# Optimization experiments

Measured on AMD Instinct MI355X. Metric: run time of the kernel, lower is better.

Reference implementation:

```python
import jax, jax.numpy as jnp
import numpy as np


def setup_inputs() -> dict:
    key = jax.random.key(0)
    k1, k2, k3 = jax.random.split(key, 3)
    B, T, H, OUT = 32, 2048, 1024, 256
    hidden_states = jax.random.normal(k1, (B, T, H), dtype=jnp.float32)
    W1 = jax.random.normal(k2, (H, H), dtype=jnp.float32) * (1.0 / np.sqrt(H))
    b1 = jnp.zeros((H,), dtype=jnp.float32)
    Wv = jax.random.normal(k3, (2 * H, OUT), dtype=jnp.float32) * (1.0 / np.sqrt(2 * H))
    bv = jnp.zeros((OUT,), dtype=jnp.float32)
    return {"hidden_states": hidden_states, "W1": W1, "b1": b1, "Wv": Wv, "bv": bv}


def reference(hidden_states, W1, b1, Wv, bv):
    # first_score = Dense(H)(hidden_states): [B,T,H]
    first_score = jnp.einsum('bth,hk->btk', hidden_states, W1) + b1
    # h_t = last timestep of the PROJECTED states: [B,H]
    h_t = first_score[:, -1, :]
    # score = dot([first_score, h_t], [2,1]): [B,T]
    score = jnp.einsum('bth,bh->bt', first_score, h_t)
    attention_weights = jax.nn.softmax(score, axis=-1)  # softmax over T
    # context = dot([hidden_states, weights], [1,1]): contract T -> [B,H]
    context_vector = jnp.einsum('bth,bt->bh', hidden_states, attention_weights)
    pre_activation = jnp.concatenate([context_vector, h_t], axis=-1)  # [B,2H]
    return jnp.tanh(pre_activation @ Wv + bv)  # [B,256]
```

## Files before the change

kernel.cpp:

```cpp
#include <hip/hip_runtime.h>
#include <math.h>

#define B   32
#define T   2048
#define H   1024
#define OUTD 256
#define NC  32
#define KC1 16

__global__ __launch_bounds__(256) void k1a_partial_ht(
    const float* __restrict__ hs, const float* __restrict__ W1,
    float* __restrict__ ph)
{
    const int tid = threadIdx.x;
    const int h   = blockIdx.x * 256 + tid;
    const int k0  = blockIdx.y * 64;

    __shared__ float s_hs[B][64];
    for (int it = 0; it < 8; ++it) {
        int idx = tid + it * 256;
        int b = idx >> 6, k = idx & 63;
        s_hs[b][k] = hs[((size_t)(b * T + (T - 1)) << 10) + k0 + k];
    }
    __syncthreads();

    float acc[B];
#pragma unroll
    for (int b = 0; b < B; ++b) acc[b] = 0.f;

    for (int k4 = 0; k4 < 16; ++k4) {
        float w0 = W1[(size_t)(k0 + k4 * 4 + 0) * H + h];
        float w1 = W1[(size_t)(k0 + k4 * 4 + 1) * H + h];
        float w2 = W1[(size_t)(k0 + k4 * 4 + 2) * H + h];
        float w3 = W1[(size_t)(k0 + k4 * 4 + 3) * H + h];
#pragma unroll
        for (int b = 0; b < B; ++b) {
            const float4 hv = *(const float4*)&s_hs[b][k4 * 4];
            acc[b] = fmaf(hv.x, w0, acc[b]);
            acc[b] = fmaf(hv.y, w1, acc[b]);
            acc[b] = fmaf(hv.z, w2, acc[b]);
            acc[b] = fmaf(hv.w, w3, acc[b]);
        }
    }
    float* dst = ph + ((size_t)blockIdx.y * B << 10);
#pragma unroll
    for (int b = 0; b < B; ++b) dst[((size_t)b << 10) + h] = acc[b];
}

__global__ __launch_bounds__(256) void k1b_reduce_ht(
    const float* __restrict__ ph, const float* __restrict__ b1,
    float* __restrict__ h_t)
{
    int i = blockIdx.x * 256 + threadIdx.x;
    int h = i & (H - 1);
    float s = b1[h];
#pragma unroll
    for (int c = 0; c < KC1; ++c)
        s += ph[((size_t)c * B << 10) + i];
    h_t[i] = s;
}

__global__ __launch_bounds__(256) void k2_compute_u(
    const float* __restrict__ W1, const float* __restrict__ h_t,
    float* __restrict__ u)
{
    const int wid  = threadIdx.x >> 6;
    const int lane = threadIdx.x & 63;
    const int k    = blockIdx.x * 4 + wid;
    const float4* wr = (const float4*)(W1 + ((size_t)k << 10));
    float4 wq[4];
#pragma unroll
    for (int j = 0; j < 4; ++j) wq[j] = wr[lane + 64 * j];

    for (int b = 0; b < B; ++b) {
        const float4* hr = (const float4*)(h_t + ((size_t)b << 10));
        float s = 0.f;
#pragma unroll
        for (int j = 0; j < 4; ++j) {
            float4 hv = hr[lane + 64 * j];
            s += wq[j].x * hv.x + wq[j].y * hv.y + wq[j].z * hv.z + wq[j].w * hv.w;
        }
#pragma unroll
        for (int off = 32; off; off >>= 1) s += __shfl_xor(s, off, 64);
        if (lane == 0) u[((size_t)b << 10) + k] = s;
    }
}

__global__ __launch_bounds__(256) void k3_fused(
    const float* __restrict__ hs, const float* __restrict__ u,
    float* __restrict__ ctx_p, float* __restrict__ m_p, float* __restrict__ l_p)
{
    const int c    = blockIdx.x;
    const int b    = blockIdx.y;
    const int w    = threadIdx.x >> 6;
    const int lane = threadIdx.x & 63;
    const int tid  = threadIdx.x;

    const float4* urow = (const float4*)(u + ((size_t)b << 10));
    float4 uq[4];
#pragma unroll
    for (int j = 0; j < 4; ++j) uq[j] = urow[lane + 64 * j];

    const int t0 = c * 64 + w * 16;
    const float4* xrow = (const float4*)(hs + ((size_t)(b * T + t0) << 10));

    float m = -INFINITY, lsum = 0.f;
    float4 acc[4];
#pragma unroll
    for (int j = 0; j < 4; ++j) acc[j] = make_float4(0.f, 0.f, 0.f, 0.f);

    float4 x[4], y[4];
#pragma unroll
    for (int j = 0; j < 4; ++j) x[j] = xrow[lane + 64 * j];

    for (int r = 0; r < 16; ++r) {
        const float4* nrow = xrow + 256;
        if (r < 15) {
#pragma unroll
            for (int j = 0; j < 4; ++j) y[j] = nrow[lane + 64 * j];
        }
        float s = 0.f;
#pragma unroll
        for (int j = 0; j < 4; ++j)
            s += x[j].x * uq[j].x + x[j].y * uq[j].y + x[j].z * uq[j].z + x[j].w * uq[j].w;
#pragma unroll
        for (int off = 32; off; off >>= 1) s += __shfl_xor(s, off, 64);

        float mn = fmaxf(m, s);
        float al = __expf(m - mn);
        float wt = __expf(s - mn);
        lsum = lsum * al + wt;
#pragma unroll
        for (int j = 0; j < 4; ++j) {
            acc[j].x = fmaf(acc[j].x, al, wt * x[j].x);
            acc[j].y = fmaf(acc[j].y, al, wt * x[j].y);
            acc[j].z = fmaf(acc[j].z, al, wt * x[j].z);
            acc[j].w = fmaf(acc[j].w, al, wt * x[j].w);
        }
        m = mn;
#pragma unroll
        for (int j = 0; j < 4; ++j) x[j] = y[j];
        xrow = nrow;
    }

    __shared__ float sm[4], sl[4];
    __shared__ float sacc[4][H];
    if (lane == 0) { sm[w] = m; sl[w] = lsum; }
    __syncthreads();
    const float mp = fmaxf(fmaxf(sm[0], sm[1]), fmaxf(sm[2], sm[3]));
    const float alw = __expf(m - mp);
    float4* sa = (float4*)&sacc[w][0];
#pragma unroll
    for (int j = 0; j < 4; ++j) {
        float4 v;
        v.x = acc[j].x * alw; v.y = acc[j].y * alw;
        v.z = acc[j].z * alw; v.w = acc[j].w * alw;
        sa[lane + 64 * j] = v;
    }
    __syncthreads();
    float lp = 0.f;
#pragma unroll
    for (int ww = 0; ww < 4; ++ww) lp += sl[ww] * __expf(sm[ww] - mp);

    float* dst = ctx_p + (((size_t)b * NC + c) << 10);
#pragma unroll
    for (int i = 0; i < 4; ++i) {
        int h = tid + 256 * i;
        dst[h] = sacc[0][h] + sacc[1][h] + sacc[2][h] + sacc[3][h];
    }
    if (tid == 0) { m_p[b * NC + c] = mp; l_p[b * NC + c] = lp; }
}

__global__ __launch_bounds__(256) void k4_combine(
    const float* __restrict__ ctx_p, const float* __restrict__ m_p,
    const float* __restrict__ l_p, const float* __restrict__ h_t,
    float* __restrict__ pre)
{
    const int b   = blockIdx.x;
    const int tid = threadIdx.x;
    __shared__ float e[NC];
    float M = -INFINITY;
    for (int c = 0; c < NC; ++c) M = fmaxf(M, m_p[b * NC + c]);
    float L = 0.f;
    for (int c = 0; c < NC; ++c) L += l_p[b * NC + c] * __expf(m_p[b * NC + c] - M);
    if (tid < NC) e[tid] = __expf(m_p[b * NC + tid] - M);
    __syncthreads();
    const float inv = 1.f / L;
#pragma unroll
    for (int i = 0; i < 4; ++i) {
        int h = tid + 256 * i;
        float s = 0.f;
#pragma unroll
        for (int c = 0; c < NC; ++c)
            s += ctx_p[(((size_t)b * NC + c) << 10) + h] * e[c];
        pre[((size_t)b << 11) + h] = s * inv;
        pre[((size_t)b << 11) + H + h] = h_t[((size_t)b << 10) + h];
    }
}

__global__ __launch_bounds__(256) void k5a_matmul(
    const float* __restrict__ pre, const float* __restrict__ Wv,
    float* __restrict__ accum)
{
    const int kc = blockIdx.x;
    const int b  = blockIdx.y;
    const int o  = threadIdx.x;
    __shared__ float sp[256];
    sp[o] = pre[((size_t)b << 11) + kc * 256 + o];
    __syncthreads();
    float acc = 0.f;
    const float* wv = Wv + (size_t)kc * 256 * OUTD + o;
#pragma unroll 8
    for (int k = 0; k < 256; ++k)
        acc = fmaf(sp[k], wv[(size_t)k * OUTD], acc);
    atomicAdd(&accum[b * OUTD + o], acc);
}

__global__ __launch_bounds__(256) void k5b_tanh(
    const float* __restrict__ accum, const float* __restrict__ bv,
    float* __restrict__ out)
{
    int i = blockIdx.x * 256 + threadIdx.x;
    out[i] = tanhf(accum[i] + bv[i & (OUTD - 1)]);
}

extern "C" void kernel_launch(void* const* d_in, const int* in_sizes, int n_in,
                              void* d_out, int out_size, void* d_ws, size_t ws_size,
                              hipStream_t stream)
{
    const float* hs = (const float*)d_in[0];
    const float* W1 = (const float*)d_in[1];
    const float* b1 = (const float*)d_in[2];
    const float* Wv = (const float*)d_in[3];
    const float* bv = (const float*)d_in[4];
    float* out = (float*)d_out;
    float* ws  = (float*)d_ws;

    float* ph    = ws;
    float* h_t   = ph + (size_t)KC1 * B * H;
    float* u     = h_t + (size_t)B * H;
    float* m_p   = u + (size_t)B * H;
    float* l_p   = m_p + B * NC;
    float* ctx_p = l_p + B * NC;
    float* pre   = ctx_p + (size_t)B * NC * H;
    float* accum = pre + (size_t)B * 2 * H;

    hipMemsetAsync(accum, 0, B * OUTD * sizeof(float), stream);

    k1a_partial_ht<<<dim3(4, KC1), 256, 0, stream>>>(hs, W1, ph);
    k1b_reduce_ht<<<(B * H) / 256, 256, 0, stream>>>(ph, b1, h_t);
    k2_compute_u<<<H / 4, 256, 0, stream>>>(W1, h_t, u);
    k3_fused<<<dim3(NC, B), 256, 0, stream>>>(hs, u, ctx_p, m_p, l_p);
    k4_combine<<<B, 256, 0, stream>>>(ctx_p, m_p, l_p, h_t, pre);
    k5a_matmul<<<dim3(8, B), 256, 0, stream>>>(pre, Wv, accum);
    k5b_tanh<<<B, 256, 0, stream>>>(accum, bv, out);
}
```

Measured before the change: 436.3 us.

## Fuse all stages into one persistent cooperative kernel with grid syncs

Merges the seven separate kernels and the memset into a single cooperative kernel. Each stage becomes a grid-stride job loop, and stages are separated by grid-wide synchronisation. The grid is sized from occupancy times CU count, and shared memory is reused across stages. This is meant to remove per-launch overhead and inter-kernel gaps, in exchange for grid-sync costs and occupancy limits from the unified register and LDS footprint.

```diff
diff --git a/kernel.cpp b/kernel.cpp
--- a/kernel.cpp
+++ b/kernel.cpp
@@ -1,227 +1,233 @@
 #include <hip/hip_runtime.h>
+#include <hip/hip_cooperative_groups.h>
 #include <math.h>
 
-#define B   32
-#define T   2048
-#define H   1024
+namespace cg = cooperative_groups;
+
+#define B    32
+#define T    2048
+#define H    1024
 #define OUTD 256
-#define NC  32
-#define KC1 16
-
-__global__ __launch_bounds__(256) void k1a_partial_ht(
+#define NC   32
+#define KC1  16
+
+__global__ __launch_bounds__(256, 4) void mega(
     const float* __restrict__ hs, const float* __restrict__ W1,
-    float* __restrict__ ph)
+    const float* __restrict__ b1, const float* __restrict__ Wv,
+    const float* __restrict__ bv, float* __restrict__ out,
+    float* ws)
 {
+    cg::grid_group grid = cg::this_grid();
+    const int bid = blockIdx.x;
     const int tid = threadIdx.x;
-    const int h   = blockIdx.x * 256 + tid;
-    const int k0  = blockIdx.y * 64;
-
-    __shared__ float s_hs[B][64];
-    for (int it = 0; it < 8; ++it) {
-        int idx = tid + it * 256;
-        int b = idx >> 6, k = idx & 63;
-        s_hs[b][k] = hs[((size_t)(b * T + (T - 1)) << 10) + k0 + k];
-    }
-    __syncthreads();
-
-    float acc[B];
-#pragma unroll
-    for (int b = 0; b < B; ++b) acc[b] = 0.f;
-
-    for (int k4 = 0; k4 < 16; ++k4) {
-        float w0 = W1[(size_t)(k0 + k4 * 4 + 0) * H + h];
-        float w1 = W1[(size_t)(k0 + k4 * 4 + 1) * H + h];
-        float w2 = W1[(size_t)(k0 + k4 * 4 + 2) * H + h];
-        float w3 = W1[(size_t)(k0 + k4 * 4 + 3) * H + h];
-#pragma unroll
+    const int gsz = gridDim.x;
+
+    float* ph    = ws;
+    float* h_t   = ph + (size_t)KC1 * B * H;
+    float* u     = h_t + (size_t)B * H;
+    float* m_p   = u + (size_t)B * H;
+    float* l_p   = m_p + B * NC;
+    float* ctx_p = l_p + B * NC;
+    float* pre   = ctx_p + (size_t)B * NC * H;
+    float* accum = pre + (size_t)B * 2 * H;
+
+    __shared__ float smem[4 * H + 8];
+
+    for (int job = bid; job < 65; job += gsz) {
+        if (job < 64) {
+            const int hh = (job & 3) * 256 + tid;
+            const int k0 = (job >> 2) * 64;
+            float (*s_hs)[64] = (float (*)[64])smem;
+            for (int it = 0; it < 8; ++it) {
+                int idx = tid + it * 256;
+                int b = idx >> 6, k = idx & 63;
+                s_hs[b][k] = hs[((size_t)(b * T + (T - 1)) << 10) + k0 + k];
+            }
+            __syncthreads();
+            float acc[B];
+#pragma unroll
+            for (int b = 0; b < B; ++b) acc[b] = 0.f;
+            for (int k4 = 0; k4 < 16; ++k4) {
+                float w0 = W1[(size_t)(k0 + k4 * 4 + 0) * H + hh];
+                float w1 = W1[(size_t)(k0 + k4 * 4 + 1) * H + hh];
+                float w2 = W1[(size_t)(k0 + k4 * 4 + 2) * H + hh];
+                float w3 = W1[(size_t)(k0 + k4 * 4 + 3) * H + hh];
+#pragma unroll
+                for (int b = 0; b < B; ++b) {
+                    const float4 hv = *(const float4*)&s_hs[b][k4 * 4];
+                    acc[b] = fmaf(hv.x, w0, acc[b]);
+                    acc[b] = fmaf(hv.y, w1, acc[b]);
+                    acc[b] = fmaf(hv.z, w2, acc[b]);
+                    acc[b] = fmaf(hv.w, w3, acc[b]);
+                }
+            }
+            float* dst = ph + ((size_t)(job >> 2) * B << 10);
+#pragma unroll
+            for (int b = 0; b < B; ++b) dst[((size_t)b << 10) + hh] = acc[b];
+            __syncthreads();
+        } else {
+            for (int i = tid; i < B * OUTD; i += 256) accum[i] = 0.f;
+        }
+    }
+    grid.sync();
+
+    for (int job = bid; job < (B * H) / 256; job += gsz) {
+        int i = job * 256 + tid;
+        int h = i & (H - 1);
+        float s = b1[h];
+#pragma unroll
+        for (int c = 0; c < KC1; ++c) s += ph[((size_t)c * B << 10) + i];
+        h_t[i] = s;
+    }
+    grid.sync();
+
+    for (int job = bid; job < H / 4; job += gsz) {
+        const int wid  = tid >> 6;
+        const int lane = tid & 63;
+        const int k    = job * 4 + wid;
+        const float4* wr = (const float4*)(W1 + ((size_t)k << 10));
+        float4 wq[4];
+#pragma unroll
+        for (int j = 0; j < 4; ++j) wq[j] = wr[lane + 64 * j];
         for (int b = 0; b < B; ++b) {
-            const float4 hv = *(const float4*)&s_hs[b][k4 * 4];
-            acc[b] = fmaf(hv.x, w0, acc[b]);
-            acc[b] = fmaf(hv.y, w1, acc[b]);
-            acc[b] = fmaf(hv.z, w2, acc[b]);
-            acc[b] = fmaf(hv.w, w3, acc[b]);
-        }
-    }
-    float* dst = ph + ((size_t)blockIdx.y * B << 10);
-#pragma unroll
-    for (int b = 0; b < B; ++b) dst[((size_t)b << 10) + h] = acc[b];
-}
-
-__global__ __launch_bounds__(256) void k1b_reduce_ht(
-    const float* __restrict__ ph, const float* __restrict__ b1,
-    float* __restrict__ h_t)
-{
-    int i = blockIdx.x * 256 + threadIdx.x;
-    int h = i & (H - 1);
-    float s = b1[h];
-#pragma unroll
-    for (int c = 0; c < KC1; ++c)
-        s += ph[((size_t)c * B << 10) + i];
-    h_t[i] = s;
-}
-
-__global__ __launch_bounds__(256) void k2_compute_u(
-    const float* __restrict__ W1, const float* __restrict__ h_t,
-    float* __restrict__ u)
-{
-    const int wid  = threadIdx.x >> 6;
-    const int lane = threadIdx.x & 63;
-    const int k    = blockIdx.x * 4 + wid;
-    const float4* wr = (const float4*)(W1 + ((size_t)k << 10));
-    float4 wq[4];
-#pragma unroll
-    for (int j = 0; j < 4; ++j) wq[j] = wr[lane + 64 * j];
-
-    for (int b = 0; b < B; ++b) {
-        const float4* hr = (const float4*)(h_t + ((size_t)b << 10));
+            const float4* hr = (const float4*)(h_t + ((size_t)b << 10));
+            float s = 0.f;
+#pragma unroll
+            for (int j = 0; j < 4; ++j) {
+                float4 hv = hr[lane + 64 * j];
+                s += wq[j].x * hv.x + wq[j].y * hv.y + wq[j].z * hv.z + wq[j].w * hv.w;
+            }
+#pragma unroll
+            for (int off = 32; off; off >>= 1) s += __shfl_xor(s, off, 64);
+            if (lane == 0) u[((size_t)b << 10) + k] = s;
+        }
+    }
+    grid.sync();
+
+    for (int cc = bid; cc < B * NC; cc += gsz) {
+        const int c    = cc & (NC - 1);
+        const int b    = cc >> 5;
+        const int w    = tid >> 6;
+        const int lane = tid & 63;
+
+        const float4* urow = (const float4*)(u + ((size_t)b << 10));
+        float4 uq[4];
+#pragma unroll
+        for (int j = 0; j < 4; ++j) uq[j] = urow[lane + 64 * j];
+
+        const int t0 = c * 64 + w * 16;
+        const float4* xrow = (const float4*)(hs + ((size_t)(b * T + t0) << 10));
+
+        float m = -INFINITY, lsum = 0.f;
+        float4 acc[4];
+#pragma unroll
+        for (int j = 0; j < 4; ++j) acc[j] = make_float4(0.f, 0.f, 0.f, 0.f);
+
+        float4 x[4], y[4];
+#pragma unroll
+        for (int j = 0; j < 4; ++j) x[j] = xrow[lane + 64 * j];
+
+        for (int r = 0; r < 16; ++r) {
+            const float4* nrow = xrow + 256;
+            if (r < 15) {
+#pragma unroll
+                for (int j = 0; j < 4; ++j) y[j] = nrow[lane + 64 * j];
+            }
+            float s = 0.f;
+#pragma unroll
+            for (int j = 0; j < 4; ++j)
+                s += x[j].x * uq[j].x + x[j].y * uq[j].y + x[j].z * uq[j].z + x[j].w * uq[j].w;
+#pragma unroll
+            for (int off = 32; off; off >>= 1) s += __shfl_xor(s, off, 64);
+
+            float mn = fmaxf(m, s);
+            float al = __expf(m - mn);
+            float wt = __expf(s - mn);
+            lsum = lsum * al + wt;
+#pragma unroll
+            for (int j = 0; j < 4; ++j) {
+                acc[j].x = fmaf(acc[j].x, al, wt * x[j].x);
+                acc[j].y = fmaf(acc[j].y, al, wt * x[j].y);
+                acc[j].z = fmaf(acc[j].z, al, wt * x[j].z);
+                acc[j].w = fmaf(acc[j].w, al, wt * x[j].w);
+            }
+            m = mn;
+#pragma unroll
+            for (int j = 0; j < 4; ++j) x[j] = y[j];
+            xrow = nrow;
+        }
+
+        float* sm = smem + 4 * H;
+        float* sl = smem + 4 * H + 4;
+        float (*sacc)[H] = (float (*)[H])smem;
+        if (lane == 0) { sm[w] = m; sl[w] = lsum; }
+        __syncthreads();
+        const float mp  = fmaxf(fmaxf(sm[0], sm[1]), fmaxf(sm[2], sm[3]));
+        const float alw = __expf(m - mp);
+        float4* sa = (float4*)&sacc[w][0];
+#pragma unroll
+        for (int j = 0; j < 4; ++j) {
+            float4 v;
+            v.x = acc[j].x * alw; v.y = acc[j].y * alw;
+            v.z = acc[j].z * alw; v.w = acc[j].w * alw;
+            sa[lane + 64 * j] = v;
+        }
+        __syncthreads();
+        float lp = 0.f;
+#pragma unroll
+        for (int ww = 0; ww < 4; ++ww) lp += sl[ww] * __expf(sm[ww] - mp);
+
+        float* dst = ctx_p + (((size_t)b * NC + c) << 10);
+#pragma unroll
+        for (int i = 0; i < 4; ++i) {
+            int h = tid + 256 * i;
+            dst[h] = sacc[0][h] + sacc[1][h] + sacc[2][h] + sacc[3][h];
+        }
+        if (tid == 0) { m_p[b * NC + c] = mp; l_p[b * NC + c] = lp; }
+        __syncthreads();
+    }
+    grid.sync();
+
+    for (int job = bid; job < B * 4; job += gsz) {
+        const int b = job >> 2;
+        const int h = (job & 3) * 256 + tid;
+        float M = -INFINITY;
+#pragma unroll
+        for (int c = 0; c < NC; ++c) M = fmaxf(M, m_p[b * NC + c]);
+        float L = 0.f;
+#pragma unroll
+        for (int c = 0; c < NC; ++c) L += l_p[b * NC + c] * __expf(m_p[b * NC + c] - M);
+        const float inv = 1.f / L;
         float s = 0.f;
 #pragma unroll
-        for (int j = 0; j < 4; ++j) {
-            float4 hv = hr[lane + 64 * j];
-            s += wq[j].x * hv.x + wq[j].y * hv.y + wq[j].z * hv.z + wq[j].w * hv.w;
-        }
-#pragma unroll
-        for (int off = 32; off; off >>= 1) s += __shfl_xor(s, off, 64);
-        if (lane == 0) u[((size_t)b << 10) + k] = s;
-    }
-}
-
-__global__ __launch_bounds__(256) void k3_fused(
-    const float* __restrict__ hs, const float* __restrict__ u,
-    float* __restrict__ ctx_p, float* __restrict__ m_p, float* __restrict__ l_p)
-{
-    const int c    = blockIdx.x;
-    const int b    = blockIdx.y;
-    const int w    = threadIdx.x >> 6;
-    const int lane = threadIdx.x & 63;
-    const int tid  = threadIdx.x;
-
-    const float4* urow = (const float4*)(u + ((size_t)b << 10));
-    float4 uq[4];
-#pragma unroll
-    for (int j = 0; j < 4; ++j) uq[j] = urow[lane + 64 * j];
-
-    const int t0 = c * 64 + w * 16;
-    const float4* xrow = (const float4*)(hs + ((size_t)(b * T + t0) << 10));
-
-    float m = -INFINITY, lsum = 0.f;
-    float4 acc[4];
-#pragma unroll
-    for (int j = 0; j < 4; ++j) acc[j] = make_float4(0.f, 0.f, 0.f, 0.f);
-
-    float4 x[4], y[4];
-#pragma unroll
-    for (int j = 0; j < 4; ++j) x[j] = xrow[lane + 64 * j];
-
-    for (int r = 0; r < 16; ++r) {
-        const float4* nrow = xrow + 256;
-        if (r < 15) {
-#pragma unroll
-            for (int j = 0; j < 4; ++j) y[j] = nrow[lane + 64 * j];
-        }
-        float s = 0.f;
-#pragma unroll
-        for (int j = 0; j < 4; ++j)
-            s += x[j].x * uq[j].x + x[j].y * uq[j].y + x[j].z * uq[j].z + x[j].w * uq[j].w;
-#pragma unroll
-        for (int off = 32; off; off >>= 1) s += __shfl_xor(s, off, 64);
-
-        float mn = fmaxf(m, s);
-        float al = __expf(m - mn);
-        float wt = __expf(s - mn);
-        lsum = lsum * al + wt;
-#pragma unroll
-        for (int j = 0; j < 4; ++j) {
-            acc[j].x = fmaf(acc[j].x, al, wt * x[j].x);
-            acc[j].y = fmaf(acc[j].y, al, wt * x[j].y);
-            acc[j].z = fmaf(acc[j].z, al, wt * x[j].z);
-            acc[j].w = fmaf(acc[j].w, al, wt * x[j].w);
-        }
-        m = mn;
-#pragma unroll
-        for (int j = 0; j < 4; ++j) x[j] = y[j];
-        xrow = nrow;
-    }
-
-    __shared__ float sm[4], sl[4];
-    __shared__ float sacc[4][H];
-    if (lane == 0) { sm[w] = m; sl[w] = lsum; }
-    __syncthreads();
-    const float mp = fmaxf(fmaxf(sm[0], sm[1]), fmaxf(sm[2], sm[3]));
-    const float alw = __expf(m - mp);
-    float4* sa = (float4*)&sacc[w][0];
-#pragma unroll
-    for (int j = 0; j < 4; ++j) {
-        float4 v;
-        v.x = acc[j].x * alw; v.y = acc[j].y * alw;
-        v.z = acc[j].z * alw; v.w = acc[j].w * alw;
-        sa[lane + 64 * j] = v;
-    }
-    __syncthreads();
-    float lp = 0.f;
-#pragma unroll
-    for (int ww = 0; ww < 4; ++ww) lp += sl[ww] * __expf(sm[ww] - mp);
-
-    float* dst = ctx_p + (((size_t)b * NC + c) << 10);
-#pragma unroll
-    for (int i = 0; i < 4; ++i) {
-        int h = tid + 256 * i;
-        dst[h] = sacc[0][h] + sacc[1][h] + sacc[2][h] + sacc[3][h];
-    }
-    if (tid == 0) { m_p[b * NC + c] = mp; l_p[b * NC + c] = lp; }
-}
-
-__global__ __launch_bounds__(256) void k4_combine(
-    const float* __restrict__ ctx_p, const float* __restrict__ m_p,
-    const float* __restrict__ l_p, const float* __restrict__ h_t,
-    float* __restrict__ pre)
-{
-    const int b   = blockIdx.x;
-    const int tid = threadIdx.x;
-    __shared__ float e[NC];
-    float M = -INFINITY;
-    for (int c = 0; c < NC; ++c) M = fmaxf(M, m_p[b * NC + c]);
-    float L = 0.f;
-    for (int c = 0; c < NC; ++c) L += l_p[b * NC + c] * __expf(m_p[b * NC + c] - M);
-    if (tid < NC) e[tid] = __expf(m_p[b * NC + tid] - M);
-    __syncthreads();
-    const float inv = 1.f / L;
-#pragma unroll
-    for (int i = 0; i < 4; ++i) {
-        int h = tid + 256 * i;
-        float s = 0.f;
-#pragma unroll
         for (int c = 0; c < NC; ++c)
-            s += ctx_p[(((size_t)b * NC + c) << 10) + h] * e[c];
+            s += ctx_p[(((size_t)b * NC + c) << 10) + h] * __expf(m_p[b * NC + c] - M);
         pre[((size_t)b << 11) + h] = s * inv;
         pre[((size_t)b << 11) + H + h] = h_t[((size_t)b << 10) + h];
     }
-}
-
-__global__ __launch_bounds__(256) void k5a_matmul(
-    const float* __restrict__ pre, const float* __restrict__ Wv,
-    float* __restrict__ accum)
-{
-    const int kc = blockIdx.x;
-    const int b  = blockIdx.y;
-    const int o  = threadIdx.x;
-    __shared__ float sp[256];
-    sp[o] = pre[((size_t)b << 11) + kc * 256 + o];
-    __syncthreads();
-    float acc = 0.f;
-    const float* wv = Wv + (size_t)kc * 256 * OUTD + o;
+    grid.sync();
+
+    for (int job = bid; job < 8 * B; job += gsz) {
+        const int kc = job & 7;
+        const int b  = job >> 3;
+        const int o  = tid;
+        float* sp = smem;
+        sp[o] = pre[((size_t)b << 11) + kc * 256 + o];
+        __syncthreads();
+        float acc = 0.f;
+        const float* wv = Wv + (size_t)kc * 256 * OUTD + o;
 #pragma unroll 8
-    for (int k = 0; k < 256; ++k)
-        acc = fmaf(sp[k], wv[(size_t)k * OUTD], acc);
-    atomicAdd(&accum[b * OUTD + o], acc);
-}
-
-__global__ __launch_bounds__(256) void k5b_tanh(
-    const float* __restrict__ accum, const float* __restrict__ bv,
-    float* __restrict__ out)
-{
-    int i = blockIdx.x * 256 + threadIdx.x;
-    out[i] = tanhf(accum[i] + bv[i & (OUTD - 1)]);
+        for (int k = 0; k < 256; ++k)
+            acc = fmaf(sp[k], wv[(size_t)k * OUTD], acc);
+        atomicAdd(&accum[b * OUTD + o], acc);
+        __syncthreads();
+    }
+    grid.sync();
+
+    for (int job = bid; job < (B * OUTD) / 256; job += gsz) {
+        int i = job * 256 + tid;
+        out[i] = tanhf(accum[i] + bv[i & (OUTD - 1)]);
+    }
 }
 
 extern "C" void kernel_launch(void* const* d_in, const int* in_sizes, int n_in,
@@ -236,22 +242,19 @@
     float* out = (float*)d_out;
     float* ws  = (float*)d_ws;
 
-    float* ph    = ws;
-    float* h_t   = ph + (size_t)KC1 * B * H;
-    float* u     = h_t + (size_t)B * H;
-    float* m_p   = u + (size_t)B * H;
-    float* l_p   = m_p + B * NC;
-    float* ctx_p = l_p + B * NC;
-    float* pre   = ctx_p + (size_t)B * NC * H;
-    float* accum = pre + (size_t)B * 2 * H;
-
-    hipMemsetAsync(accum, 0, B * OUTD * sizeof(float), stream);
-
-    k1a_partial_ht<<<dim3(4, KC1), 256, 0, stream>>>(hs, W1, ph);
-    k1b_reduce_ht<<<(B * H) / 256, 256, 0, stream>>>(ph, b1, h_t);
-    k2_compute_u<<<H / 4, 256, 0, stream>>>(W1, h_t, u);
-    k3_fused<<<dim3(NC, B), 256, 0, stream>>>(hs, u, ctx_p, m_p, l_p);
-    k4_combine<<<B, 256, 0, stream>>>(ctx_p, m_p, l_p, h_t, pre);
-    k5a_matmul<<<dim3(8, B), 256, 0, stream>>>(pre, Wv, accum);
-    k5b_tanh<<<B, 256, 0, stream>>>(accum, bv, out);
+    static int coop_grid = 0;
+    if (coop_grid == 0) {
+        int dev = 0, ncu = 0, nb = 0;
+        (void)hipGetDevice(&dev);
+        (void)hipDeviceGetAttribute(&ncu, hipDeviceAttributeMultiprocessorCount, dev);
+        (void)hipOccupancyMaxActiveBlocksPerMultiprocessor(&nb, mega, 256, 0);
+        int g = nb * ncu;
+        if (g <= 0 || g > 1024) g = 1024;
+        coop_grid = g;
+    }
+
+    void* args[] = { (void*)&hs, (void*)&W1, (void*)&b1, (void*)&Wv,
+                     (void*)&bv, (void*)&out, (void*)&ws };
+    (void)hipLaunchCooperativeKernel(mega, dim3(coop_grid), dim3(256),
+                                     args, 0, stream);
 }
```

Result: slower. 736.2 us (+68.8%).
